# Optimization experiments

Measured on AMD Instinct MI355X. Metric: run time of the kernel, lower is better.

Reference implementation:

```python
import jax, jax.numpy as jnp
import numpy as np

T, B, E, H = 1024, 2, 1024, 16
D = E // H


def setup_inputs() -> dict:
    key = jax.random.key(0)
    ks = jax.random.split(key, 5)
    s = 1.0 / np.sqrt(E)  # xavier_uniform bound ~ sqrt(6/(fan_in+fan_out)); scale suffices for a numeric baseline
    return {
        "query": jax.random.normal(ks[0], (T, B, E), jnp.float32),
        "key_": jax.random.normal(ks[1], (T, B, E), jnp.float32),
        "value": jax.random.normal(ks[2], (T, B, E), jnp.float32),
        "in_proj_weight": jax.random.uniform(ks[3], (3 * E, E), jnp.float32, -s, s),
        "in_proj_bias": jnp.zeros((3 * E,), jnp.float32),
        "out_proj_weight": jax.random.uniform(ks[4], (E, E), jnp.float32, -s, s),
        "out_proj_bias": jnp.zeros((E,), jnp.float32),
    }


def reference(query, key_, value, in_proj_weight, in_proj_bias, out_proj_weight, out_proj_bias):
    # Faithful to CumulativeLinearMultiheadAttentionKV.forward with
    # batch_first=False, is_causal=True, no padding mask, no kv cache.
    Tl, Bl, El = query.shape
    wq, wk, wv = jnp.split(in_proj_weight, 3, axis=0)
    bq, bk, bv = jnp.split(in_proj_bias, 3)
    q = query @ wq.T + bq          # (T, B, E)
    k = key_ @ wk.T + bk
    v = value @ wv.T + bv

    def to_bhtd(x):
        return x.reshape(Tl, Bl, H, D).transpose(1, 2, 0, 3)  # (B, H, T, D)

    q, k, v = to_bhtd(q), to_bhtd(k), to_bhtd(v)

    scale = 1.0 / np.sqrt(D)  # SDPA-style default scale (scale=None)
    # cumulative linear attention: prefix sums of k_s \otimes v_s
    kv = jnp.einsum('bhsk,bhsv->bhskv', k, v)        # (B, H, T, D, D)
    kv_store = jnp.cumsum(kv, axis=2)                # causal KV state per step
    out = jnp.einsum('bhtk,bhtkv->bhtv', q, kv_store) * scale  # (B, H, T, D)

    out = out.transpose(2, 0, 1, 3).reshape(Tl, Bl, El)  # back to (T, B, E)
    out = out @ out_proj_weight.T + out_proj_bias
    return out
```

## Files before the change

kernel.cpp:

```cpp
#include <hip/hip_runtime.h>


#define E_DIM 1024

typedef short bf16x8 __attribute__((ext_vector_type(8)));
typedef float f32x4  __attribute__((ext_vector_type(4)));

__device__ inline unsigned short f2bf(float f) {
    unsigned u = __builtin_bit_cast(unsigned, f);
    u = (u + 0x7FFFu + ((u >> 16) & 1u)) >> 16;
    return (unsigned short)u;
}

__device__ inline void gload_lds16(const void* g, void* l) {
    __builtin_amdgcn_global_load_lds(
        (const __attribute__((address_space(1))) unsigned int*)g,
        (__attribute__((address_space(3))) unsigned int*)l, 16, 0, 0);
}

__global__ __launch_bounds__(256) void k_cast(
    const float* __restrict__ q_in, const float* __restrict__ k_in,
    const float* __restrict__ v_in, const float* __restrict__ w_in,
    const float* __restrict__ w_out, unsigned short* __restrict__ dst)
{
    #pragma unroll
    for (int l = 0; l < 4; ++l) {
        int id8 = blockIdx.x * 256 + threadIdx.x + l * 327680;
        const float* src;
        if (id8 < 262144)        src = q_in  + (size_t)id8 * 8;
        else if (id8 < 524288)   src = k_in  + (size_t)(id8 - 262144) * 8;
        else if (id8 < 786432)   src = v_in  + (size_t)(id8 - 524288) * 8;
        else if (id8 < 1179648)  src = w_in  + (size_t)(id8 - 786432) * 8;
        else                     src = w_out + (size_t)(id8 - 1179648) * 8;
        float4 f0 = *reinterpret_cast<const float4*>(src);
        float4 f1 = *reinterpret_cast<const float4*>(src + 4);
        ushort4 o0, o1;
        o0.x = f2bf(f0.x); o0.y = f2bf(f0.y); o0.z = f2bf(f0.z); o0.w = f2bf(f0.w);
        o1.x = f2bf(f1.x); o1.y = f2bf(f1.y); o1.z = f2bf(f1.z); o1.w = f2bf(f1.w);
        *reinterpret_cast<ushort4*>(dst + (size_t)id8 * 8)     = o0;
        *reinterpret_cast<ushort4*>(dst + (size_t)id8 * 8 + 4) = o1;
    }
}

__global__ __launch_bounds__(256) void k_gin(
    const unsigned short* __restrict__ xbf, const unsigned short* __restrict__ Wibf,
    const float* __restrict__ b_in,
    unsigned short* __restrict__ qslab, unsigned short* __restrict__ kslab,
    unsigned short* __restrict__ vtb)
{
    const int i = blockIdx.x;
    const int tile = (i & 7) * 96 + (i >> 3);
    const int x = tile & 7, y = (tile >> 3) & 31, z = tile >> 8;

    const unsigned short* X = xbf + (size_t)z * 2097152;
    const unsigned short* W = Wibf + (size_t)z * 1048576;
    const float* bz = b_in + z * E_DIM;

    const int nBase = x * 128;
    const int mBase = y * 64;
    const int b = mBase >> 10, tBase = mBase & 1023;

    __shared__ short As[2][64 * 64];
    __shared__ short Bs[2][128 * 64];

    const int tid = threadIdx.x;
    const int lane = tid & 63, wave = tid >> 6;
    const int wr = wave >> 1, wc = wave & 1;
    const int l15 = lane & 15, l4 = lane >> 4;

    auto stageAB = [&](int bufI, int k0) {
        #pragma unroll
        for (int l = 0; l < 4; ++l) {
            int off = l * 4096 + tid * 16;
            int row = off >> 7, kb = off & 127;
            gload_lds16((const char*)W + ((size_t)(nBase + row) * E_DIM + k0) * 2 + kb,
                        (char*)&Bs[bufI][0] + off);
        }
        #pragma unroll
        for (int l = 0; l < 2; ++l) {
            int off = l * 4096 + tid * 16;
            int row = off >> 7, kb = off & 127;
            gload_lds16((const char*)X +
                            ((size_t)((tBase + row) * 2 + b) * E_DIM + k0) * 2 + kb,
                        (char*)&As[bufI][0] + off);
        }
    };

    f32x4 acc[2][4] = {};

    stageAB(0, 0);
    __syncthreads();
    int cur = 0;
    for (int it = 0; it < 16; ++it) {
        if (it < 15) stageAB(cur ^ 1, (it + 1) * 64);
        #pragma unroll
        for (int kk = 0; kk < 64; kk += 32) {
            bf16x8 af[2], bfr[4];
            #pragma unroll
            for (int ii = 0; ii < 2; ++ii)
                af[ii] = *reinterpret_cast<const bf16x8*>(
                            &As[cur][(wr * 32 + ii * 16 + l15) * 64 + kk + l4 * 8]);
            #pragma unroll
            for (int j = 0; j < 4; ++j)
                bfr[j] = *reinterpret_cast<const bf16x8*>(
                            &Bs[cur][(wc * 64 + j * 16 + l15) * 64 + kk + l4 * 8]);
            #pragma unroll
            for (int ii = 0; ii < 2; ++ii)
                #pragma unroll
                for (int j = 0; j < 4; ++j)
                    acc[ii][j] = __builtin_amdgcn_mfma_f32_16x16x32_bf16(
                        af[ii], bfr[j], acc[ii][j], 0, 0, 0);
        }
        __syncthreads();
        cur ^= 1;
    }

    #pragma unroll
    for (int ii = 0; ii < 2; ++ii) {
        int t0 = tBase + wr * 32 + ii * 16 + l4 * 4;
        #pragma unroll
        for (int j = 0; j < 4; ++j) {
            int col = nBase + wc * 64 + j * 16 + l15;
            float bv = bz[col];
            unsigned short v4[4];
            #pragma unroll
            for (int q = 0; q < 4; ++q) v4[q] = f2bf(acc[ii][j][q] + bv);
            if (z == 0) {
                #pragma unroll
                for (int q = 0; q < 4; ++q)
                    qslab[(size_t)b * 1048576 + (size_t)(t0 + q) * E_DIM + col] = v4[q];
            } else if (z == 1) {
                #pragma unroll
                for (int q = 0; q < 4; ++q)
                    kslab[(size_t)b * 1048576 + (size_t)(t0 + q) * E_DIM + col] = v4[q];
            } else {
                ushort4 w = {v4[0], v4[1], v4[2], v4[3]};
                *reinterpret_cast<ushort4*>(
                    &vtb[((size_t)b * 1024 + col) * 1024 + t0]) = w;
            }
        }
    }
}

__global__ __launch_bounds__(256) void k_attn(
    const unsigned short* __restrict__ qslab, const unsigned short* __restrict__ kslab,
    const unsigned short* __restrict__ vtb, unsigned short* __restrict__ attnbf)
{
    const int i = blockIdx.x;
    const int xcd = i & 7, u = i >> 3;
    const int bh = xcd * 4 + (u >> 4);
    const int qtr = u & 15;
    const int qt = ((u >> 5) & 1) ? (15 - qtr) : qtr;
    const int b = bh >> 4, h = bh & 15;
    const int colb = h * 64, t0q = qt * 64;

    __shared__ short Qs[64 * 64];
    __shared__ short Ks[2][64 * 64];
    __shared__ short Vts[2][64 * 64];
    __shared__ short Ss[64 * 72];

    const int tid = threadIdx.x;
    const int lane = tid & 63, wave = tid >> 6;
    const int wr = wave >> 1, wc = wave & 1;
    const int l15 = lane & 15, l4 = lane >> 4;

    auto stageKV = [&](int bufI, int c) {
        int t0k = c * 64;
        #pragma unroll
        for (int l = 0; l < 2; ++l) {
            int off = l * 4096 + tid * 16;
            int row = off >> 7, kb = off & 127;
            gload_lds16((const char*)kslab +
                            ((size_t)b * 1048576 + (size_t)(t0k + row) * E_DIM + colb) * 2 + kb,
                        (char*)&Ks[bufI][0] + off);
            gload_lds16((const char*)vtb +
                            (((size_t)(b * 1024 + colb + row)) * 1024 + t0k) * 2 + kb,
                        (char*)&Vts[bufI][0] + off);
        }
    };

    #pragma unroll
    for (int l = 0; l < 2; ++l) {
        int off = l * 4096 + tid * 16;
        int row = off >> 7, kb = off & 127;
        gload_lds16((const char*)qslab +
                        ((size_t)b * 1048576 + (size_t)(t0q + row) * E_DIM + colb) * 2 + kb,
                    (char*)Qs + off);
    }
    stageKV(0, 0);
    __syncthreads();

    f32x4 oacc[2][2] = {};
    int cur = 0;

    for (int c = 0; c <= qt; ++c) {
        if (c < qt) stageKV(cur ^ 1, c + 1);

        f32x4 sacc[2][2] = {};
        #pragma unroll
        for (int kk = 0; kk < 64; kk += 32) {
            bf16x8 af[2], bfr[2];
            #pragma unroll
            for (int ii = 0; ii < 2; ++ii)
                af[ii] = *reinterpret_cast<const bf16x8*>(
                            &Qs[(wr * 32 + ii * 16 + l15) * 64 + kk + l4 * 8]);
            #pragma unroll
            for (int j = 0; j < 2; ++j)
                bfr[j] = *reinterpret_cast<const bf16x8*>(
                            &Ks[cur][(wc * 32 + j * 16 + l15) * 64 + kk + l4 * 8]);
            #pragma unroll
            for (int ii = 0; ii < 2; ++ii)
                #pragma unroll
                for (int j = 0; j < 2; ++j)
                    sacc[ii][j] = __builtin_amdgcn_mfma_f32_16x16x32_bf16(
                        af[ii], bfr[j], sacc[ii][j], 0, 0, 0);
        }
        const bool diag = (c == qt);
        #pragma unroll
        for (int ii = 0; ii < 2; ++ii) {
            #pragma unroll
            for (int j = 0; j < 2; ++j) {
                int kr = wc * 32 + j * 16 + l15;
                #pragma unroll
                for (int q = 0; q < 4; ++q) {
                    int qr = wr * 32 + ii * 16 + l4 * 4 + q;
                    short sv = (short)f2bf(sacc[ii][j][q]);
                    Ss[qr * 72 + kr] = (!diag || kr <= qr) ? sv : (short)0;
                }
            }
        }
        __syncthreads();

        #pragma unroll
        for (int kk = 0; kk < 64; kk += 32) {
            bf16x8 af[2], bfr[2];
            #pragma unroll
            for (int ii = 0; ii < 2; ++ii)
                af[ii] = *reinterpret_cast<const bf16x8*>(
                            &Ss[(wr * 32 + ii * 16 + l15) * 72 + kk + l4 * 8]);
            #pragma unroll
            for (int j = 0; j < 2; ++j)
                bfr[j] = *reinterpret_cast<const bf16x8*>(
                            &Vts[cur][(wc * 32 + j * 16 + l15) * 64 + kk + l4 * 8]);
            #pragma unroll
            for (int ii = 0; ii < 2; ++ii)
                #pragma unroll
                for (int j = 0; j < 2; ++j)
                    oacc[ii][j] = __builtin_amdgcn_mfma_f32_16x16x32_bf16(
                        af[ii], bfr[j], oacc[ii][j], 0, 0, 0);
        }
        __syncthreads();
        cur ^= 1;
    }

    #pragma unroll
    for (int ii = 0; ii < 2; ++ii) {
        #pragma unroll
        for (int j = 0; j < 2; ++j) {
            int dv = wc * 32 + j * 16 + l15;
            #pragma unroll
            for (int q = 0; q < 4; ++q) {
                int qr = wr * 32 + ii * 16 + l4 * 4 + q;
                attnbf[(size_t)b * 1048576 + (size_t)(t0q + qr) * E_DIM + colb + dv] =
                    f2bf(oacc[ii][j][q] * 0.125f);
            }
        }
    }
}

__global__ __launch_bounds__(256) void k_gout(
    const unsigned short* __restrict__ attnbf, const unsigned short* __restrict__ Wobf,
    const float* __restrict__ bias, float* __restrict__ out)
{
    const int i = blockIdx.x;
    const int tile = (i & 7) * 64 + (i >> 3);
    const int x = tile & 15, y = tile >> 4;
    const int nBase = x * 64;
    const int mBase = y * 64;

    __shared__ short As[2][64 * 64];
    __shared__ short Bs[2][64 * 64];

    const int tid = threadIdx.x;
    const int lane = tid & 63, wave = tid >> 6;
    const int wr = wave >> 1, wc = wave & 1;
    const int l15 = lane & 15, l4 = lane >> 4;

    auto stage = [&](int bufI, int k0) {
        #pragma unroll
        for (int l = 0; l < 2; ++l) {
            int off = l * 4096 + tid * 16;
            int row = off >> 7, kb = off & 127;
            gload_lds16((const char*)Wobf + ((size_t)(nBase + row) * E_DIM + k0) * 2 + kb,
                        (char*)&Bs[bufI][0] + off);
            int r = mBase + row, t = r >> 1, bb = r & 1;
            gload_lds16((const char*)attnbf +
                            ((size_t)bb * 1048576 + (size_t)t * E_DIM + k0) * 2 + kb,
                        (char*)&As[bufI][0] + off);
        }
    };

    f32x4 acc[2][2] = {};

    stage(0, 0);
    __syncthreads();
    int cur = 0;
    for (int it = 0; it < 16; ++it) {
        if (it < 15) stage(cur ^ 1, (it + 1) * 64);
        #pragma unroll
        for (int kk = 0; kk < 64; kk += 32) {
            bf16x8 af[2], bfr[2];
            #pragma unroll
            for (int ii = 0; ii < 2; ++ii)
                af[ii] = *reinterpret_cast<const bf16x8*>(
                            &As[cur][(wr * 32 + ii * 16 + l15) * 64 + kk + l4 * 8]);
            #pragma unroll
            for (int j = 0; j < 2; ++j)
                bfr[j] = *reinterpret_cast<const bf16x8*>(
                            &Bs[cur][(wc * 32 + j * 16 + l15) * 64 + kk + l4 * 8]);
            #pragma unroll
            for (int ii = 0; ii < 2; ++ii)
                #pragma unroll
                for (int j = 0; j < 2; ++j)
                    acc[ii][j] = __builtin_amdgcn_mfma_f32_16x16x32_bf16(
                        af[ii], bfr[j], acc[ii][j], 0, 0, 0);
        }
        __syncthreads();
        cur ^= 1;
    }

    #pragma unroll
    for (int ii = 0; ii < 2; ++ii) {
        int r0 = mBase + wr * 32 + ii * 16 + l4 * 4;
        #pragma unroll
        for (int j = 0; j < 2; ++j) {
            int col = nBase + wc * 32 + j * 16 + l15;
            float bv = bias[col];
            #pragma unroll
            for (int q = 0; q < 4; ++q)
                out[(size_t)(r0 + q) * E_DIM + col] = acc[ii][j][q] + bv;
        }
    }
}

extern "C" void kernel_launch(void* const* d_in, const int* in_sizes, int n_in,
                              void* d_out, int out_size, void* d_ws, size_t ws_size,
                              hipStream_t stream)
{
    const float* q_in  = (const float*)d_in[0];
    const float* k_in  = (const float*)d_in[1];
    const float* v_in  = (const float*)d_in[2];
    const float* w_in  = (const float*)d_in[3];
    const float* b_in  = (const float*)d_in[4];
    const float* w_out = (const float*)d_in[5];
    const float* b_out = (const float*)d_in[6];

    char* w = (char*)d_ws;
    unsigned short* xbf    = (unsigned short*)w;
    unsigned short* Wibf   = (unsigned short*)(w + 12582912);
    unsigned short* Wobf   = (unsigned short*)(w + 18874368);
    unsigned short* qslab  = (unsigned short*)(w + 20971520);
    unsigned short* kslab  = (unsigned short*)(w + 25165824);
    unsigned short* vtb    = (unsigned short*)(w + 29360128);
    unsigned short* attnbf = (unsigned short*)(w + 33554432);
    float* outp = (float*)d_out;

    k_cast<<<1280, 256, 0, stream>>>(q_in, k_in, v_in, w_in, w_out, xbf);
    k_gin<<<768, 256, 0, stream>>>(xbf, Wibf, b_in, qslab, kslab, vtb);
    k_attn<<<512, 256, 0, stream>>>(qslab, kslab, vtb, attnbf);
    k_gout<<<512, 256, 0, stream>>>(attnbf, Wobf, b_out, outp);
}
```

Before: 154.0 us.

## Fuse activation bf16 cast into input GEMM, widen N tile, swizzle LDS layouts

Drops the separate cast pass over the activations. The input projection GEMM now loads fp32 query/key/value rows, converts them to bf16 in registers and writes them to LDS, so the bf16 activation copy is never written to or read back from global memory. The input GEMM tile widens from 128 to 256 output columns, which halves the grid and doubles accumulators per wave. An XOR swizzle on LDS rows is applied across all GEMM and attention tiles to reduce bank conflicts on the fragment reads. In exchange there is more register pressure, fewer blocks in the input GEMM, and synchronous fp32 global loads in its staging path.

```diff
diff --git a/kernel.cpp b/kernel.cpp
--- a/kernel.cpp
+++ b/kernel.cpp
@@ -18,96 +18,109 @@
         (__attribute__((address_space(3))) unsigned int*)l, 16, 0, 0);
 }
 
-__global__ __launch_bounds__(256) void k_cast(
+__device__ inline int swzb(int row, int colbyte) {
+    return colbyte ^ ((row & 7) << 4);
+}
+
+__global__ __launch_bounds__(256) void k_castw(
+    const float* __restrict__ w_in, const float* __restrict__ w_out,
+    unsigned short* __restrict__ dst)
+{
+    const int id8 = blockIdx.x * 256 + threadIdx.x;
+    const int WI8 = 3 * E_DIM * E_DIM / 8;
+    const float* src = (id8 < WI8) ? (w_in + (size_t)id8 * 8)
+                                   : (w_out + (size_t)(id8 - WI8) * 8);
+    float4 f0 = *reinterpret_cast<const float4*>(src);
+    float4 f1 = *reinterpret_cast<const float4*>(src + 4);
+    ushort4 o0, o1;
+    o0.x = f2bf(f0.x); o0.y = f2bf(f0.y); o0.z = f2bf(f0.z); o0.w = f2bf(f0.w);
+    o1.x = f2bf(f1.x); o1.y = f2bf(f1.y); o1.z = f2bf(f1.z); o1.w = f2bf(f1.w);
+    *reinterpret_cast<ushort4*>(dst + (size_t)id8 * 8)     = o0;
+    *reinterpret_cast<ushort4*>(dst + (size_t)id8 * 8 + 4) = o1;
+}
+
+__global__ __launch_bounds__(256) void k_gin(
     const float* __restrict__ q_in, const float* __restrict__ k_in,
-    const float* __restrict__ v_in, const float* __restrict__ w_in,
-    const float* __restrict__ w_out, unsigned short* __restrict__ dst)
-{
-    #pragma unroll
-    for (int l = 0; l < 4; ++l) {
-        int id8 = blockIdx.x * 256 + threadIdx.x + l * 327680;
-        const float* src;
-        if (id8 < 262144)        src = q_in  + (size_t)id8 * 8;
-        else if (id8 < 524288)   src = k_in  + (size_t)(id8 - 262144) * 8;
-        else if (id8 < 786432)   src = v_in  + (size_t)(id8 - 524288) * 8;
-        else if (id8 < 1179648)  src = w_in  + (size_t)(id8 - 786432) * 8;
-        else                     src = w_out + (size_t)(id8 - 1179648) * 8;
-        float4 f0 = *reinterpret_cast<const float4*>(src);
-        float4 f1 = *reinterpret_cast<const float4*>(src + 4);
-        ushort4 o0, o1;
-        o0.x = f2bf(f0.x); o0.y = f2bf(f0.y); o0.z = f2bf(f0.z); o0.w = f2bf(f0.w);
-        o1.x = f2bf(f1.x); o1.y = f2bf(f1.y); o1.z = f2bf(f1.z); o1.w = f2bf(f1.w);
-        *reinterpret_cast<ushort4*>(dst + (size_t)id8 * 8)     = o0;
-        *reinterpret_cast<ushort4*>(dst + (size_t)id8 * 8 + 4) = o1;
-    }
-}
-
-__global__ __launch_bounds__(256) void k_gin(
-    const unsigned short* __restrict__ xbf, const unsigned short* __restrict__ Wibf,
+    const float* __restrict__ v_in, const unsigned short* __restrict__ Wibf,
     const float* __restrict__ b_in,
     unsigned short* __restrict__ qslab, unsigned short* __restrict__ kslab,
     unsigned short* __restrict__ vtb)
 {
     const int i = blockIdx.x;
-    const int tile = (i & 7) * 96 + (i >> 3);
-    const int x = tile & 7, y = (tile >> 3) & 31, z = tile >> 8;
-
-    const unsigned short* X = xbf + (size_t)z * 2097152;
+    const int tile = (i & 7) * 48 + (i >> 3);
+    const int z = tile >> 7;
+    const int rem = tile & 127;
+    const int x = rem >> 5, y = rem & 31;
+
+    const float* X = (z == 0) ? q_in : (z == 1 ? k_in : v_in);
     const unsigned short* W = Wibf + (size_t)z * 1048576;
     const float* bz = b_in + z * E_DIM;
 
-    const int nBase = x * 128;
+    const int nBase = x * 256;
     const int mBase = y * 64;
     const int b = mBase >> 10, tBase = mBase & 1023;
 
     __shared__ short As[2][64 * 64];
-    __shared__ short Bs[2][128 * 64];
+    __shared__ short Bs[2][256 * 64];
 
     const int tid = threadIdx.x;
     const int lane = tid & 63, wave = tid >> 6;
     const int wr = wave >> 1, wc = wave & 1;
     const int l15 = lane & 15, l4 = lane >> 4;
 
-    auto stageAB = [&](int bufI, int k0) {
-        #pragma unroll
-        for (int l = 0; l < 4; ++l) {
+    auto stage = [&](int bufI, int k0) {
+        #pragma unroll
+        for (int l = 0; l < 8; ++l) {
             int off = l * 4096 + tid * 16;
-            int row = off >> 7, kb = off & 127;
-            gload_lds16((const char*)W + ((size_t)(nBase + row) * E_DIM + k0) * 2 + kb,
+            int row = off >> 7, cb = off & 127;
+            gload_lds16((const char*)W + ((size_t)(nBase + row) * E_DIM + k0) * 2
+                            + swzb(row, cb),
                         (char*)&Bs[bufI][0] + off);
         }
         #pragma unroll
         for (int l = 0; l < 2; ++l) {
-            int off = l * 4096 + tid * 16;
-            int row = off >> 7, kb = off & 127;
-            gload_lds16((const char*)X +
-                            ((size_t)((tBase + row) * 2 + b) * E_DIM + k0) * 2 + kb,
-                        (char*)&As[bufI][0] + off);
+            int u = tid + 256 * l;
+            int row = u >> 3, cslot = u & 7;
+            const float* src = &X[(size_t)((tBase + row) * 2 + b) * E_DIM
+                                  + k0 + cslot * 8];
+            float4 f0 = *reinterpret_cast<const float4*>(src);
+            float4 f1 = *reinterpret_cast<const float4*>(src + 4);
+            bf16x8 p;
+            p[0] = (short)f2bf(f0.x); p[1] = (short)f2bf(f0.y);
+            p[2] = (short)f2bf(f0.z); p[3] = (short)f2bf(f0.w);
+            p[4] = (short)f2bf(f1.x); p[5] = (short)f2bf(f1.y);
+            p[6] = (short)f2bf(f1.z); p[7] = (short)f2bf(f1.w);
+            *reinterpret_cast<bf16x8*>(
+                &As[bufI][row * 64 + (swzb(row, cslot * 16) >> 1)]) = p;
         }
     };
 
-    f32x4 acc[2][4] = {};
-
-    stageAB(0, 0);
+    f32x4 acc[2][8] = {};
+
+    stage(0, 0);
     __syncthreads();
     int cur = 0;
     for (int it = 0; it < 16; ++it) {
-        if (it < 15) stageAB(cur ^ 1, (it + 1) * 64);
+        if (it < 15) stage(cur ^ 1, (it + 1) * 64);
         #pragma unroll
         for (int kk = 0; kk < 64; kk += 32) {
-            bf16x8 af[2], bfr[4];
-            #pragma unroll
-            for (int ii = 0; ii < 2; ++ii)
+            bf16x8 af[2], bfr[8];
+            #pragma unroll
+            for (int ii = 0; ii < 2; ++ii) {
+                int row = wr * 32 + ii * 16 + l15;
                 af[ii] = *reinterpret_cast<const bf16x8*>(
-                            &As[cur][(wr * 32 + ii * 16 + l15) * 64 + kk + l4 * 8]);
-            #pragma unroll
-            for (int j = 0; j < 4; ++j)
+                    &As[cur][row * 64 + (swzb(row, (kk + l4 * 8) * 2) >> 1)]);
+            }
+            #pragma unroll
+            for (int j = 0; j < 8; ++j) {
+                int row = wc * 128 + j * 16 + l15;
                 bfr[j] = *reinterpret_cast<const bf16x8*>(
-                            &Bs[cur][(wc * 64 + j * 16 + l15) * 64 + kk + l4 * 8]);
-            #pragma unroll
-            for (int ii = 0; ii < 2; ++ii)
-                #pragma unroll
-                for (int j = 0; j < 4; ++j)
+                    &Bs[cur][row * 64 + (swzb(row, (kk + l4 * 8) * 2) >> 1)]);
+            }
+            #pragma unroll
+            for (int ii = 0; ii < 2; ++ii)
+                #pragma unroll
+                for (int j = 0; j < 8; ++j)
                     acc[ii][j] = __builtin_amdgcn_mfma_f32_16x16x32_bf16(
                         af[ii], bfr[j], acc[ii][j], 0, 0, 0);
         }
@@ -119,8 +132,8 @@
     for (int ii = 0; ii < 2; ++ii) {
         int t0 = tBase + wr * 32 + ii * 16 + l4 * 4;
         #pragma unroll
-        for (int j = 0; j < 4; ++j) {
-            int col = nBase + wc * 64 + j * 16 + l15;
+        for (int j = 0; j < 8; ++j) {
+            int col = nBase + wc * 128 + j * 16 + l15;
             float bv = bz[col];
             unsigned short v4[4];
             #pragma unroll
@@ -169,12 +182,13 @@
         #pragma unroll
         for (int l = 0; l < 2; ++l) {
             int off = l * 4096 + tid * 16;
-            int row = off >> 7, kb = off & 127;
+            int row = off >> 7, cb = off & 127;
+            int scb = swzb(row, cb);
             gload_lds16((const char*)kslab +
-                            ((size_t)b * 1048576 + (size_t)(t0k + row) * E_DIM + colb) * 2 + kb,
+                            ((size_t)b * 1048576 + (size_t)(t0k + row) * E_DIM + colb) * 2 + scb,
                         (char*)&Ks[bufI][0] + off);
             gload_lds16((const char*)vtb +
-                            (((size_t)(b * 1024 + colb + row)) * 1024 + t0k) * 2 + kb,
+                            (((size_t)(b * 1024 + colb + row)) * 1024 + t0k) * 2 + scb,
                         (char*)&Vts[bufI][0] + off);
         }
     };
@@ -182,9 +196,10 @@
     #pragma unroll
     for (int l = 0; l < 2; ++l) {
         int off = l * 4096 + tid * 16;
-        int row = off >> 7, kb = off & 127;
+        int row = off >> 7, cb = off & 127;
         gload_lds16((const char*)qslab +
-                        ((size_t)b * 1048576 + (size_t)(t0q + row) * E_DIM + colb) * 2 + kb,
+                        ((size_t)b * 1048576 + (size_t)(t0q + row) * E_DIM + colb) * 2
+                        + swzb(row, cb),
                     (char*)Qs + off);
     }
     stageKV(0, 0);
@@ -201,13 +216,17 @@
         for (int kk = 0; kk < 64; kk += 32) {
             bf16x8 af[2], bfr[2];
             #pragma unroll
-            for (int ii = 0; ii < 2; ++ii)
+            for (int ii = 0; ii < 2; ++ii) {
+                int row = wr * 32 + ii * 16 + l15;
                 af[ii] = *reinterpret_cast<const bf16x8*>(
-                            &Qs[(wr * 32 + ii * 16 + l15) * 64 + kk + l4 * 8]);
-            #pragma unroll
-            for (int j = 0; j < 2; ++j)
+                    &Qs[row * 64 + (swzb(row, (kk + l4 * 8) * 2) >> 1)]);
+            }
+            #pragma unroll
+            for (int j = 0; j < 2; ++j) {
+                int row = wc * 32 + j * 16 + l15;
                 bfr[j] = *reinterpret_cast<const bf16x8*>(
-                            &Ks[cur][(wc * 32 + j * 16 + l15) * 64 + kk + l4 * 8]);
+                    &Ks[cur][row * 64 + (swzb(row, (kk + l4 * 8) * 2) >> 1)]);
+            }
             #pragma unroll
             for (int ii = 0; ii < 2; ++ii)
                 #pragma unroll
@@ -239,9 +258,11 @@
                 af[ii] = *reinterpret_cast<const bf16x8*>(
                             &Ss[(wr * 32 + ii * 16 + l15) * 72 + kk + l4 * 8]);
             #pragma unroll
-            for (int j = 0; j < 2; ++j)
+            for (int j = 0; j < 2; ++j) {
+                int row = wc * 32 + j * 16 + l15;
                 bfr[j] = *reinterpret_cast<const bf16x8*>(
-                            &Vts[cur][(wc * 32 + j * 16 + l15) * 64 + kk + l4 * 8]);
+                    &Vts[cur][row * 64 + (swzb(row, (kk + l4 * 8) * 2) >> 1)]);
+            }
             #pragma unroll
             for (int ii = 0; ii < 2; ++ii)
                 #pragma unroll
@@ -290,12 +311,13 @@
         #pragma unroll
         for (int l = 0; l < 2; ++l) {
             int off = l * 4096 + tid * 16;
-            int row = off >> 7, kb = off & 127;
-            gload_lds16((const char*)Wobf + ((size_t)(nBase + row) * E_DIM + k0) * 2 + kb,
+            int row = off >> 7, cb = off & 127;
+            int scb = swzb(row, cb);
+            gload_lds16((const char*)Wobf + ((size_t)(nBase + row) * E_DIM + k0) * 2 + scb,
                         (char*)&Bs[bufI][0] + off);
             int r = mBase + row, t = r >> 1, bb = r & 1;
             gload_lds16((const char*)attnbf +
-                            ((size_t)bb * 1048576 + (size_t)t * E_DIM + k0) * 2 + kb,
+                            ((size_t)bb * 1048576 + (size_t)t * E_DIM + k0) * 2 + scb,
                         (char*)&As[bufI][0] + off);
         }
     };
@@ -311,13 +333,17 @@
         for (int kk = 0; kk < 64; kk += 32) {
             bf16x8 af[2], bfr[2];
             #pragma unroll
-            for (int ii = 0; ii < 2; ++ii)
+            for (int ii = 0; ii < 2; ++ii) {
+                int row = wr * 32 + ii * 16 + l15;
                 af[ii] = *reinterpret_cast<const bf16x8*>(
-                            &As[cur][(wr * 32 + ii * 16 + l15) * 64 + kk + l4 * 8]);
-            #pragma unroll
-            for (int j = 0; j < 2; ++j)
+                    &As[cur][row * 64 + (swzb(row, (kk + l4 * 8) * 2) >> 1)]);
+            }
+            #pragma unroll
+            for (int j = 0; j < 2; ++j) {
+                int row = wc * 32 + j * 16 + l15;
                 bfr[j] = *reinterpret_cast<const bf16x8*>(
-                            &Bs[cur][(wc * 32 + j * 16 + l15) * 64 + kk + l4 * 8]);
+                    &Bs[cur][row * 64 + (swzb(row, (kk + l4 * 8) * 2) >> 1)]);
+            }
             #pragma unroll
             for (int ii = 0; ii < 2; ++ii)
                 #pragma unroll
@@ -356,17 +382,16 @@
     const float* b_out = (const float*)d_in[6];
 
     char* w = (char*)d_ws;
-    unsigned short* xbf    = (unsigned short*)w;
-    unsigned short* Wibf   = (unsigned short*)(w + 12582912);
-    unsigned short* Wobf   = (unsigned short*)(w + 18874368);
-    unsigned short* qslab  = (unsigned short*)(w + 20971520);
-    unsigned short* kslab  = (unsigned short*)(w + 25165824);
-    unsigned short* vtb    = (unsigned short*)(w + 29360128);
-    unsigned short* attnbf = (unsigned short*)(w + 33554432);
+    unsigned short* Wibf   = (unsigned short*)w;
+    unsigned short* Wobf   = (unsigned short*)(w + 6291456);
+    unsigned short* qslab  = (unsigned short*)(w + 8388608);
+    unsigned short* kslab  = (unsigned short*)(w + 12582912);
+    unsigned short* vtb    = (unsigned short*)(w + 16777216);
+    unsigned short* attnbf = (unsigned short*)(w + 20971520);
     float* outp = (float*)d_out;
 
-    k_cast<<<1280, 256, 0, stream>>>(q_in, k_in, v_in, w_in, w_out, xbf);
-    k_gin<<<768, 256, 0, stream>>>(xbf, Wibf, b_in, qslab, kslab, vtb);
+    k_castw<<<2048, 256, 0, stream>>>(w_in, w_out, Wibf);
+    k_gin<<<384, 256, 0, stream>>>(q_in, k_in, v_in, Wibf, b_in, qslab, kslab, vtb);
     k_attn<<<512, 256, 0, stream>>>(qslab, kslab, vtb, attnbf);
     k_gout<<<512, 256, 0, stream>>>(attnbf, Wobf, b_out, outp);
 }
```

Result: no change. 155.5 us (+1.0%).
